# Optimization experiments

Hardware: AMD Instinct MI355X
Metric: run time of the kernel (lower is better)

## Reference

```python
import jax, jax.numpy as jnp
import numpy as np

H = 1024          # hidden_size
NH = 16           # num_heads = hidden_size // head_dim
DK = 64           # head_dim (key)
DV = 64           # head_v_dim
VDIM = 1024       # value_dim
DECAY_LR, GATE_LR, A_LR, V_LR = 64, 160, 64, 64
W_SCALE = -0.6065306597126334  # -exp(-0.5)
GN_EPS = 64 * 1e-5             # head_dim * norm_eps


def _lora(x, A, B, b, act):
    h = x @ A.T
    if act is not None:
        h = act(h)
    y = h @ B.T
    return y if b is None else y + b


def setup_inputs() -> dict:
    key = jax.random.key(0)
    ks = iter(jax.random.split(key, 40))
    def n(shape, s=0.02):
        return jax.random.normal(next(ks), shape, dtype=jnp.float32) * s
    inp = {
        'hidden_states': jax.random.normal(next(ks), (8, 2048, H), jnp.float32),
        'v_first': jax.random.normal(next(ks), (8, 2048, VDIM), jnp.float32),
        'x_r': n((1, 1, H), 0.5), 'x_w': n((1, 1, H), 0.5), 'x_k': n((1, 1, H), 0.5),
        'x_v': n((1, 1, H), 0.5), 'x_a': n((1, 1, H), 0.5), 'x_g': n((1, 1, H), 0.5),
        'k_k': 0.71 + n((H,), 0.05),
        'k_a': 1.02 + n((H,), 0.05),
        'r_k': -0.04 + n((NH, DK), 0.05),
        'W_r': n((H, H)), 'W_k': n((H, H)), 'W_v': n((VDIM, H)), 'W_o': n((H, VDIM)),
        'w_lora_A': n((DECAY_LR, H)), 'w_lora_B': n((H, DECAY_LR)), 'w_lora_b': n((H,), 0.5) - 4.0,
        'a_lora_A': n((A_LR, H)), 'a_lora_B': n((H, A_LR)), 'a_lora_b': n((H,), 0.1),
        'v_lora_A': n((V_LR, H)), 'v_lora_B': n((VDIM, V_LR)), 'v_lora_b': 0.73 + n((VDIM,), 0.1),
        'g_lora_A': n((GATE_LR, H)), 'g_lora_B': n((VDIM, GATE_LR)),
        'gn_w': jnp.ones((VDIM,), jnp.float32), 'gn_b': jnp.zeros((VDIM,), jnp.float32),
    }
    return inp


def reference(hidden_states, v_first, x_r, x_w, x_k, x_v, x_a, x_g, k_k, k_a, r_k,
              W_r, W_k, W_v, W_o, w_lora_A, w_lora_B, w_lora_b,
              a_lora_A, a_lora_B, a_lora_b, v_lora_A, v_lora_B, v_lora_b,
              g_lora_A, g_lora_B, gn_w, gn_b):
    x = hidden_states
    B_, T, _ = x.shape
    # token shift: delta[t] = x[t-1] - x[t], x[-1] = 0
    shifted = jnp.pad(x, ((0, 0), (1, 0), (0, 0)))[:, :T]
    delta = shifted - x
    xr = x + delta * x_r; xw = x + delta * x_w; xk = x + delta * x_k
    xv = x + delta * x_v; xa = x + delta * x_a; xg = x + delta * x_g

    r = xr @ W_r.T
    w = W_SCALE * jax.nn.sigmoid(_lora(xw, w_lora_A, w_lora_B, w_lora_b, jnp.tanh))  # log-decay in (-e^-0.5, 0)
    k = xk @ W_k.T
    v = xv @ W_v.T
    v = v + (v_first - v) * jax.nn.sigmoid(_lora(xv, v_lora_A, v_lora_B, v_lora_b, None))  # layer_idx != 0
    a = jax.nn.sigmoid(_lora(xa, a_lora_A, a_lora_B, a_lora_b, None))
    g = _lora(xg, g_lora_A, g_lora_B, None, jax.nn.sigmoid)

    kk = (k * k_k).reshape(B_, T, NH, DK)
    kk = kk / jnp.maximum(jnp.linalg.norm(kk, axis=-1, keepdims=True), 1e-12)  # l2 norm per head
    k = k * (1.0 + (a - 1.0) * k_a)

    rh = r.reshape(B_, T, NH, DK)
    wh = w.reshape(B_, T, NH, DK)
    kh = k.reshape(B_, T, NH, DK)
    vh = v.reshape(B_, T, NH, DV)
    ah = -kk                               # delta-rule 'a' (removal direction)
    bh = kk * a.reshape(B_, T, NH, DK)     # delta-rule 'b' (write direction)

    def step(S, inputs):
        # S: [B, H, DK, DV]; inputs each [B, H, D]
        r_t, w_t, k_t, v_t, a_t, b_t = inputs
        sa = jnp.einsum('bhk,bhkv->bhv', a_t, S)
        S = S * jnp.exp(w_t)[..., None] \
            + jnp.einsum('bhk,bhv->bhkv', b_t, sa) \
            + jnp.einsum('bhk,bhv->bhkv', k_t, v_t)
        o_t = jnp.einsum('bhk,bhkv->bhv', r_t, S)
        return S, o_t

    seq = tuple(jnp.moveaxis(t, 1, 0) for t in (rh, wh, kh, vh, ah, bh))  # [T,B,H,D]
    S0 = jnp.zeros((B_, NH, DK, DV), dtype=x.dtype)
    _, o = jax.lax.scan(step, S0, seq)
    o = jnp.moveaxis(o, 0, 1)  # [B, T, NH, DV]

    # GroupNorm with num_groups = num_heads over value_dim channels == per-head LayerNorm (no per-head affine)
    mu = o.mean(-1, keepdims=True)
    var = o.var(-1, keepdims=True)
    on = ((o - mu) / jnp.sqrt(var + GN_EPS)).reshape(B_, T, VDIM) * gn_w + gn_b

    bonus = ((rh * kh * r_k).sum(-1, keepdims=True) * vh).reshape(B_, T, VDIM)
    out = ((on + bonus) * g) @ W_o.T
    return out
```

## Files before the change

kernel.cpp:

```cpp
#include <hip/hip_runtime.h>
#include <hip/hip_bf16.h>


#define DEVI __device__ __forceinline__

constexpr int TSEQ = 2048;
constexpr int HID  = 1024;
constexpr int BTOT = 16384;
constexpr int CCH  = 32;
constexpr int NCH  = TSEQ / CCH;
constexpr float W_SCALE = -0.6065306597126334f;
constexpr float GN_EPS  = 6.4e-4f;

using s16x8  = __attribute__((ext_vector_type(8))) short;
using f32x4v = __attribute__((ext_vector_type(4))) float;

DEVI float4 ld4(const float* p) { return *reinterpret_cast<const float4*>(p); }
DEVI void   st4(float* p, float4 v) { *reinterpret_cast<float4*>(p) = v; }
DEVI float  sigf(float x) { return 1.0f / (1.0f + __expf(-x)); }
DEVI unsigned short bfr(float f) {
    unsigned int u = __float_as_uint(f);
    return (unsigned short)((u + 0x7fffu + ((u >> 16) & 1u)) >> 16);
}
DEVI float bff(unsigned short s) { return __uint_as_float(((unsigned int)s) << 16); }
DEVI unsigned int pk2(float lo, float hi) {
    return ((unsigned int)bfr(hi) << 16) | (unsigned int)bfr(lo);
}
DEVI f32x4v MF(s16x8 a, s16x8 b, f32x4v c) {
    return __builtin_amdgcn_mfma_f32_16x16x32_bf16(a, b, c, 0, 0, 0);
}
DEVI void gl16(const void* g, void* l) {
    __builtin_amdgcn_global_load_lds(
        (const __attribute__((address_space(1))) unsigned int*)g,
        (__attribute__((address_space(3))) unsigned int*)l, 16, 0, 0);
}
DEVI void gl4(const void* g, void* l) {
    __builtin_amdgcn_global_load_lds(
        (const __attribute__((address_space(1))) unsigned int*)g,
        (__attribute__((address_space(3))) unsigned int*)l, 4, 0, 0);
}

__global__ __launch_bounds__(256) void cast_kernel(
        const float* __restrict__ s, unsigned short* __restrict__ d, int n) {
    int i = (blockIdx.x * 256 + threadIdx.x) * 4;
    if (i >= n) return;
    float4 v = ld4(s + i);
    ushort4 o; o.x = bfr(v.x); o.y = bfr(v.y); o.z = bfr(v.z); o.w = bfr(v.w);
    *reinterpret_cast<ushort4*>(d + i) = o;
}

__global__ __launch_bounds__(256) void proj3_kernel(
        const float* __restrict__ x,
        const float* __restrict__ cr, const float* __restrict__ ck,
        const float* __restrict__ cv,
        const unsigned short* __restrict__ Wr, const unsigned short* __restrict__ Wk,
        const unsigned short* __restrict__ Wv,
        unsigned short* __restrict__ Ro, unsigned short* __restrict__ Ko,
        unsigned short* __restrict__ Vo) {
    __shared__ __align__(16) unsigned short As[3][64 * 32];
    __shared__ __align__(16) unsigned short Bs[3][128 * 32];
    const int tid = threadIdx.x;
    const int w = tid >> 6, l = tid & 63;
    const int bm = blockIdx.x * 64, bn = blockIdx.y * 128;
    const int wm = w >> 1, wn = w & 1;
    const int lr = l & 15, lq = l >> 4, lk = lq * 8;

    f32x4v acc[3][2][4];
#pragma unroll
    for (int p = 0; p < 3; p++)
#pragma unroll
        for (int i = 0; i < 2; i++)
#pragma unroll
            for (int j = 0; j < 4; j++)
#pragma unroll
                for (int q = 0; q < 4; q++) acc[p][i][j][q] = 0.f;

    const float* cvs[3] = {cr, ck, cv};
    const unsigned short* Ws[3] = {Wr, Wk, Wv};

    for (int k0 = 0; k0 < HID; k0 += 32) {
        {
            const int row = tid >> 2, kp = (tid & 3) * 8;
            const int gr = bm + row;
            const float* xp = x + (size_t)gr * HID + k0 + kp;
            float4 x0 = ld4(xp), x1 = ld4(xp + 4);
            float4 p0 = make_float4(0.f, 0.f, 0.f, 0.f), p1 = p0;
            if ((gr & (TSEQ - 1)) != 0) { p0 = ld4(xp - HID); p1 = ld4(xp - HID + 4); }
            float xb[8] = {x0.x, x0.y, x0.z, x0.w, x1.x, x1.y, x1.z, x1.w};
            float dx[8] = {p0.x - x0.x, p0.y - x0.y, p0.z - x0.z, p0.w - x0.w,
                           p1.x - x1.x, p1.y - x1.y, p1.z - x1.z, p1.w - x1.w};
#pragma unroll
            for (int p = 0; p < 3; p++) {
                float4 c0 = ld4(cvs[p] + k0 + kp), c1 = ld4(cvs[p] + k0 + kp + 4);
                float cc[8] = {c0.x, c0.y, c0.z, c0.w, c1.x, c1.y, c1.z, c1.w};
                uint4 u;
                u.x = pk2(fmaf(dx[0], cc[0], xb[0]), fmaf(dx[1], cc[1], xb[1]));
                u.y = pk2(fmaf(dx[2], cc[2], xb[2]), fmaf(dx[3], cc[3], xb[3]));
                u.z = pk2(fmaf(dx[4], cc[4], xb[4]), fmaf(dx[5], cc[5], xb[5]));
                u.w = pk2(fmaf(dx[6], cc[6], xb[6]), fmaf(dx[7], cc[7], xb[7]));
                *reinterpret_cast<uint4*>(&As[p][row * 32 + kp]) = u;
            }
        }
#pragma unroll
        for (int p = 0; p < 3; p++)
#pragma unroll
            for (int c = 0; c < 2; c++) {
                int idx = c * 256 + tid;
                int rw = idx >> 2, kp2 = (idx & 3) * 8;
                gl16(Ws[p] + (size_t)(bn + rw) * HID + k0 + kp2,
                     &Bs[p][c * 2048 + w * 512]);
            }
        __syncthreads();
#pragma unroll
        for (int p = 0; p < 3; p++) {
            s16x8 af[2], bf4[4];
#pragma unroll
            for (int i = 0; i < 2; i++)
                af[i] = *reinterpret_cast<const s16x8*>(
                    &As[p][(wm * 32 + i * 16 + lr) * 32 + lk]);
#pragma unroll
            for (int j = 0; j < 4; j++)
                bf4[j] = *reinterpret_cast<const s16x8*>(
                    &Bs[p][(wn * 64 + j * 16 + lr) * 32 + lk]);
#pragma unroll
            for (int i = 0; i < 2; i++)
#pragma unroll
                for (int j = 0; j < 4; j++)
                    acc[p][i][j] = MF(af[i], bf4[j], acc[p][i][j]);
        }
        __syncthreads();
    }

    unsigned short* dsts[3] = {Ro, Ko, Vo};
#pragma unroll
    for (int p = 0; p < 3; p++)
#pragma unroll
        for (int i = 0; i < 2; i++)
#pragma unroll
            for (int j = 0; j < 4; j++)
#pragma unroll
                for (int q = 0; q < 4; q++) {
                    const int grow = bm + wm * 32 + i * 16 + lq * 4 + q;
                    const int gcol = bn + wn * 64 + j * 16 + lr;
                    dsts[p][(size_t)grow * HID + gcol] = bfr(acc[p][i][j][q]);
                }
}

template<int BM, int BN, int MODE, bool MIXA, bool OUTBF>
__global__ __launch_bounds__(256) void mgemm(
        const void* __restrict__ Ap, const float* __restrict__ cvec,
        const unsigned short* __restrict__ Bw, void* Cout,
        int N, int K,
        const float* __restrict__ bias,
        const unsigned short* aux1, const float* __restrict__ aux2) {
    constexpr int BK = 32;
    constexpr int WM_ = (BN == 128) ? 2 : (BM == 128 ? 4 : 2);
    constexpr int WN_ = (BN == 128) ? 2 : (BM == 128 ? 1 : 2);
    constexpr int WTM = BM / WM_, WTN = BN / WN_;
    constexpr int MF_ = WTM / 16, NF = WTN / 16;
    constexpr int ACALLS = (BM * BK) / 2048;
    constexpr int BCALLS = (BN * BK) / 2048;
    __shared__ __align__(16) unsigned short As[BM * BK];
    __shared__ __align__(16) unsigned short Bs[BN * BK];
    const int tid = threadIdx.x;
    const int w = tid >> 6, l = tid & 63;
    const int bm = blockIdx.x * BM, bn = blockIdx.y * BN;
    const int wm = w / WN_, wn = w % WN_;
    const int lr = l & 15, lk = (l >> 4) * 8;

    f32x4v acc[MF_][NF];
#pragma unroll
    for (int i = 0; i < MF_; i++)
#pragma unroll
        for (int j = 0; j < NF; j++)
#pragma unroll
            for (int q = 0; q < 4; q++) acc[i][j][q] = 0.f;

    for (int k0 = 0; k0 < K; k0 += BK) {
        if (MIXA) {
            const float* Axf = (const float*)Ap;
#pragma unroll
            for (int c = 0; c < ACALLS; c++) {
                int idx = c * 256 + tid;
                int row = idx >> 2, kp = (idx & 3) * 8;
                int gr = bm + row;
                const float* xp = Axf + (size_t)gr * K + k0 + kp;
                float4 x0 = ld4(xp), x1 = ld4(xp + 4);
                float4 p0 = make_float4(0.f,0.f,0.f,0.f), p1 = p0;
                if ((gr & (TSEQ - 1)) != 0) { p0 = ld4(xp - HID); p1 = ld4(xp - HID + 4); }
                float4 c0 = ld4(cvec + k0 + kp), c1 = ld4(cvec + k0 + kp + 4);
                uint4 u;
                u.x = pk2(fmaf(p0.x - x0.x, c0.x, x0.x), fmaf(p0.y - x0.y, c0.y, x0.y));
                u.y = pk2(fmaf(p0.z - x0.z, c0.z, x0.z), fmaf(p0.w - x0.w, c0.w, x0.w));
                u.z = pk2(fmaf(p1.x - x1.x, c1.x, x1.x), fmaf(p1.y - x1.y, c1.y, x1.y));
                u.w = pk2(fmaf(p1.z - x1.z, c1.z, x1.z), fmaf(p1.w - x1.w, c1.w, x1.w));
                *reinterpret_cast<uint4*>(&As[idx * 8]) = u;
            }
        } else {
            const unsigned short* Ab = (const unsigned short*)Ap;
#pragma unroll
            for (int c = 0; c < ACALLS; c++) {
                int idx = c * 256 + tid;
                int row = idx >> 2, kp = (idx & 3) * 8;
                gl16(Ab + (size_t)(bm + row) * K + k0 + kp, &As[c * 2048 + w * 512]);
            }
        }
#pragma unroll
        for (int c = 0; c < BCALLS; c++) {
            int idx = c * 256 + tid;
            int row = idx >> 2, kp = (idx & 3) * 8;
            int gc = bn + row; if (gc > N - 1) gc = N - 1;
            gl16(Bw + (size_t)gc * K + k0 + kp, &Bs[c * 2048 + w * 512]);
        }
        __syncthreads();
        s16x8 afx[MF_], bfx[NF];
#pragma unroll
        for (int i = 0; i < MF_; i++)
            afx[i] = *reinterpret_cast<const s16x8*>(&As[(wm * WTM + i * 16 + lr) * BK + lk]);
#pragma unroll
        for (int j = 0; j < NF; j++)
            bfx[j] = *reinterpret_cast<const s16x8*>(&Bs[(wn * WTN + j * 16 + lr) * BK + lk]);
#pragma unroll
        for (int i = 0; i < MF_; i++)
#pragma unroll
            for (int j = 0; j < NF; j++)
                acc[i][j] = __builtin_amdgcn_mfma_f32_16x16x32_bf16(
                    afx[i], bfx[j], acc[i][j], 0, 0, 0);
        __syncthreads();
    }

#pragma unroll
    for (int i = 0; i < MF_; i++) {
        const int grow0 = bm + wm * WTM + i * 16 + (l >> 4) * 4;
#pragma unroll
        for (int j = 0; j < NF; j++) {
            const int gcol = bn + wn * WTN + j * 16 + lr;
            if (gcol >= N) continue;
            const float bsv = (MODE >= 3) ? bias[gcol] : 0.f;
#pragma unroll
            for (int q = 0; q < 4; q++) {
                const int grow = grow0 + q;
                float d = acc[i][j][q];
                if (MODE == 1) d = tanhf(d);
                else if (MODE == 2) d = sigf(d);
                else if (MODE == 3) d = __expf(W_SCALE * sigf(d + bsv));
                else if (MODE == 4) d = sigf(d + bsv);
                else if (MODE == 5) {
                    float v0 = bff(aux1[(size_t)grow * N + gcol]);
                    d = fmaf(aux2[(size_t)grow * N + gcol] - v0, sigf(d + bsv), v0);
                }
                else if (MODE == 6) d = W_SCALE * sigf(d + bsv);
                if (OUTBF) ((unsigned short*)Cout)[(size_t)grow * N + gcol] = bfr(d);
                else       ((float*)Cout)[(size_t)grow * N + gcol] = d;
            }
        }
    }
}

__global__ __launch_bounds__(64) void cprep_kernel(
        unsigned short* __restrict__ K16, unsigned short* __restrict__ A16,
        unsigned short* __restrict__ R16, unsigned short* __restrict__ KK16,
        const unsigned short* __restrict__ W16,
        const float* __restrict__ kkc, const float* __restrict__ kac,
        const float* __restrict__ rkw,
        float* __restrict__ SB, float* __restrict__ Ed,
        unsigned short* __restrict__ MvH, unsigned short* __restrict__ MvL) {
    __shared__ __align__(16) unsigned short sA[32][64], sB[32][64];
    __shared__ __align__(16) float Mab[32][36];
    const int bid = blockIdx.x;
    const int bh = bid >> 6, ch = bid & 63;
    const int bb = bh >> 4, hh = bh & 15;
    const int l = threadIdx.x;
    const int chn = hh * 64 + l;
    const float kkcv = kkc[chn], kacv = kac[chn], rkv = rkw[chn];
    size_t off = ((size_t)(bb * TSEQ) + ch * CCH) * HID + chn;
    float cw = 0.f, er = 1.f;
    for (int i = 0; i < CCH; i++, off += HID) {
        const float k = bff(K16[off]);
        const float a = bff(A16[off]);
        const float r = bff(R16[off]);
        const float wv = bff(W16[off]);
        const float kr = k * kkcv;
        float ss = kr * kr;
        ss += __shfl_xor(ss, 1);  ss += __shfl_xor(ss, 2);
        ss += __shfl_xor(ss, 4);  ss += __shfl_xor(ss, 8);
        ss += __shfl_xor(ss, 16); ss += __shfl_xor(ss, 32);
        const float inv = 1.0f / fmaxf(sqrtf(ss), 1e-12f);
        const float kk = kr * inv;
        const float b  = kk * a;
        const float kn = k * fmaf(a - 1.0f, kacv, 1.0f);
        float s3 = r * kn * rkv;
        s3 += __shfl_xor(s3, 1);  s3 += __shfl_xor(s3, 2);
        s3 += __shfl_xor(s3, 4);  s3 += __shfl_xor(s3, 8);
        s3 += __shfl_xor(s3, 16); s3 += __shfl_xor(s3, 32);
        if (l == 0) SB[(size_t)bh * TSEQ + ch * CCH + i] = s3;
        const float cwp = cw; cw += wv;
        const float ea = __expf(cwp), ei = __expf(-cw);
        er = __expf(cw);
        const unsigned short At = bfr(-kk * ea);
        const unsigned short Bt = bfr(b * ei);
        KK16[off] = At;
        A16[off]  = Bt;
        K16[off]  = bfr(kn * ei);
        R16[off]  = bfr(r * er);
        sA[i][l] = At; sB[i][l] = Bt;
    }
    Ed[((size_t)bh * NCH + ch) * 64 + l] = er;
    __syncthreads();
    const int lr = l & 15, lq = l >> 4;
    f32x4v z4; z4[0] = z4[1] = z4[2] = z4[3] = 0.f;
#pragma unroll
    for (int mi = 0; mi < 2; mi++)
#pragma unroll
        for (int ni = 0; ni < 2; ni++) {
            s16x8 a0 = *reinterpret_cast<const s16x8*>(&sA[mi * 16 + lr][lq * 8]);
            s16x8 a1 = *reinterpret_cast<const s16x8*>(&sA[mi * 16 + lr][32 + lq * 8]);
            s16x8 b0 = *reinterpret_cast<const s16x8*>(&sB[ni * 16 + lr][lq * 8]);
            s16x8 b1 = *reinterpret_cast<const s16x8*>(&sB[ni * 16 + lr][32 + lq * 8]);
            f32x4v m = MF(a1, b1, MF(a0, b0, z4));
#pragma unroll
            for (int q = 0; q < 4; q++) {
                int r = mi * 16 + lq * 4 + q, cc2 = ni * 16 + lr;
                Mab[r][cc2] = (cc2 < r) ? m[q] : 0.f;
            }
        }
    __syncthreads();
    const int j = l & 31;
    float m[32];
#pragma unroll
    for (int i = 0; i < 32; i++) m[i] = (i == j) ? 1.f : 0.f;
#pragma unroll
    for (int i = 1; i < 32; i++) {
        float p0 = 0.f, p1 = 0.f, p2 = 0.f, p3 = 0.f;
#pragma unroll
        for (int k4_ = 0; k4_ < 32; k4_ += 4) {
            if (k4_ >= i) break;
            float4 L4 = *reinterpret_cast<const float4*>(&Mab[i][k4_]);
            p0 = fmaf(L4.x, m[k4_ + 0], p0);
            if (k4_ + 1 < i) p1 = fmaf(L4.y, m[k4_ + 1], p1);
            if (k4_ + 2 < i) p2 = fmaf(L4.z, m[k4_ + 2], p2);
            if (k4_ + 3 < i) p3 = fmaf(L4.w, m[k4_ + 3], p3);
        }
        m[i] += (p0 + p1) + (p2 + p3);
    }
    if (l < 32) {
        unsigned short* dH = MvH + (size_t)(bh * NCH + ch) * 1024;
        unsigned short* dL = MvL + (size_t)(bh * NCH + ch) * 1024;
#pragma unroll
        for (int i = 0; i < 32; i++) {
            unsigned short h = bfr(m[i]);
            dH[i * 32 + j] = h;
            dL[i * 32 + j] = bfr(m[i] - bff(h));
        }
    }
}

__global__ __launch_bounds__(256) void recchunk_kernel(
        const unsigned short* __restrict__ AtG, const unsigned short* __restrict__ BtG,
        const unsigned short* __restrict__ KtG, const unsigned short* __restrict__ RtG,
        const unsigned short* __restrict__ V16, const float* __restrict__ Ed,
        const unsigned short* __restrict__ MvH, const unsigned short* __restrict__ MvL,
        float* __restrict__ Ob) {
    __shared__ __align__(16) unsigned short stT[2][4][CCH][64];
    __shared__ __align__(16) unsigned short stMh[2][32][32], stMl[2][32][32];
    __shared__ __align__(16) unsigned short stV[2][CCH][16];
    __shared__ __align__(16) float stEd[2][64];
    __shared__ __align__(16) unsigned short Shi[16][74], Slo[16][74];
    __shared__ __align__(16) unsigned short BtT[64][42], KtT[64][42];
    __shared__ __align__(16) unsigned short VT[16][42];
    __shared__ __align__(16) unsigned short MakH[32][42], MakL[32][42];
    __shared__ __align__(16) unsigned short MrkH[32][42], MrkL[32][42];
    __shared__ __align__(16) unsigned short MrbH[32][42], MrbL[32][42];
    __shared__ __align__(16) unsigned short rhTH[16][42], rhTL[16][42];

    const int bid = blockIdx.x;
    const int vq = bid >> 7, bh = bid & 127;
    const int tid = threadIdx.x;
    const int w = tid >> 6, l = tid & 63;
    const int lr = l & 15, lq = l >> 4;
    const int bb = bh >> 4, hh = bh & 15;
    const size_t rowoff = ((size_t)bb * TSEQ) * HID + hh * 64;
    const int mi = w >> 1, ni = w & 1;

    const int r8 = l >> 3, ck = l & 7;
    const int swz8 = (ck ^ r8) * 8;

    auto STAGE = [&](int buf, int cn) {
        if (cn >= NCH) return;
        const size_t cb = rowoff + (size_t)(cn * CCH) * HID;
        const unsigned short* srcs[4] = {AtG, BtG, KtG, RtG};
        const unsigned short* T = srcs[w];
#pragma unroll
        for (int c = 0; c < 4; c++)
            gl16(T + cb + (size_t)(c * 8 + r8) * HID + swz8, &stT[buf][w][c * 8][0]);
        if (w == 0) {
            gl16(V16 + cb + (size_t)(l >> 1) * HID + vq * 16 + (l & 1) * 8,
                 &stV[buf][0][0]);
            gl4(Ed + ((size_t)bh * NCH + cn) * 64 + l, &stEd[buf][0]);
        } else if (w == 1) {
#pragma unroll
            for (int c = 0; c < 2; c++)
                gl16(MvH + (size_t)(bh * NCH + cn) * 1024 + c * 512 + l * 8,
                     (char*)&stMh[buf][0][0] + c * 1024);
        } else if (w == 2) {
#pragma unroll
            for (int c = 0; c < 2; c++)
                gl16(MvL + (size_t)(bh * NCH + cn) * 1024 + c * 512 + l * 8,
                     (char*)&stMl[buf][0][0] + c * 1024);
        }
    };

    for (int idx = tid; idx < 16 * 74; idx += 256) {
        ((unsigned short*)Shi)[idx] = 0;
        ((unsigned short*)Slo)[idx] = 0;
    }
    STAGE(0, 0);
    asm volatile("s_waitcnt vmcnt(0)" ::: "memory");
    __syncthreads();

    auto fragT = [&](int bf, int tn, int rbase, int kb) -> s16x8 {
        int row = rbase + lr;
        int chv = ((kb >> 3) + lq) ^ (row & 7);
        return *reinterpret_cast<const s16x8*>(
            (const char*)&stT[bf][tn][0][0] + row * 128 + chv * 16);
    };
    auto fragS = [&](const unsigned short (*Sx)[74], int kb) -> s16x8 {
        return *reinterpret_cast<const s16x8*>(&Sx[lr][kb + lq * 8]);
    };
    auto frag42 = [&](const unsigned short (*T)[42], int rbase) -> s16x8 {
        return *reinterpret_cast<const s16x8*>(&T[rbase + lr][lq * 8]);
    };

    f32x4v Sacc;
#pragma unroll
    for (int q = 0; q < 4; q++) Sacc[q] = 0.f;
    f32x4v z4; z4[0] = z4[1] = z4[2] = z4[3] = 0.f;

    int buf = 0;
    for (int c = 0; c < NCH; c++) {
        STAGE(buf ^ 1, c + 1);
        {
            const int tt = tid & 31, g8 = tid >> 5;
            const int ch = g8 ^ (tt & 7);
            uint4 bu = *reinterpret_cast<const uint4*>(&stT[buf][1][tt][ch * 8]);
            uint4 ku = *reinterpret_cast<const uint4*>(&stT[buf][2][tt][ch * 8]);
            unsigned int bw[4] = {bu.x, bu.y, bu.z, bu.w};
            unsigned int kw[4] = {ku.x, ku.y, ku.z, ku.w};
#pragma unroll
            for (int e = 0; e < 4; e++) {
                BtT[g8 * 8 + 2 * e][tt]     = (unsigned short)(bw[e] & 0xffffu);
                BtT[g8 * 8 + 2 * e + 1][tt] = (unsigned short)(bw[e] >> 16);
                KtT[g8 * 8 + 2 * e][tt]     = (unsigned short)(kw[e] & 0xffffu);
                KtT[g8 * 8 + 2 * e + 1][tt] = (unsigned short)(kw[e] >> 16);
            }
            if (g8 < 4) {
                ushort4 vu = *reinterpret_cast<const ushort4*>(&stV[buf][tt][g8 * 4]);
                VT[g8 * 4 + 0][tt] = vu.x; VT[g8 * 4 + 1][tt] = vu.y;
                VT[g8 * 4 + 2][tt] = vu.z; VT[g8 * 4 + 3][tt] = vu.w;
            }
        }
        s16x8 atm0 = fragT(buf, 0, mi * 16, 0), atm1 = fragT(buf, 0, mi * 16, 32);
        s16x8 rt0  = fragT(buf, 3, mi * 16, 0), rt1  = fragT(buf, 3, mi * 16, 32);
        s16x8 bt0  = fragT(buf, 1, ni * 16, 0), bt1  = fragT(buf, 1, ni * 16, 32);
        s16x8 kt0  = fragT(buf, 2, ni * 16, 0), kt1  = fragT(buf, 2, ni * 16, 32);
        f32x4v mak = MF(atm1, kt1, MF(atm0, kt0, z4));
        f32x4v mrk = MF(rt1, kt1, MF(rt0, kt0, z4));
        f32x4v mrb = MF(rt1, bt1, MF(rt0, bt0, z4));
        f32x4v oac = z4, rhT = z4;
        {
            s16x8 sh0 = fragS(Shi, 0), sh1 = fragS(Shi, 32);
            s16x8 sl0 = fragS(Slo, 0), sl1 = fragS(Slo, 32);
            if (ni == 0) {
                oac = MF(rt1, sl1, MF(rt0, sl0, MF(rt1, sh1, MF(rt0, sh0, z4))));
            } else {
                rhT = MF(sl1, atm1, MF(sl0, atm0, MF(sh1, atm1, MF(sh0, atm0, z4))));
            }
        }
#pragma unroll
        for (int q = 0; q < 4; q++) {
            const int r = mi * 16 + lq * 4 + q, cc = ni * 16 + lr;
            float vv = (cc < r) ? mak[q] : 0.f;
            unsigned short h = bfr(vv);
            MakH[r][cc] = h; MakL[r][cc] = bfr(vv - bff(h));
            vv = (cc <= r) ? mrk[q] : 0.f; h = bfr(vv);
            MrkH[r][cc] = h; MrkL[r][cc] = bfr(vv - bff(h));
            vv = (cc <= r) ? mrb[q] : 0.f; h = bfr(vv);
            MrbH[r][cc] = h; MrbL[r][cc] = bfr(vv - bff(h));
        }
        __syncthreads();
        {
            s16x8 vt0 = frag42(VT, 0);
            if (ni == 0) {
                oac = MF(frag42(MrkL, mi * 16), vt0,
                         MF(frag42(MrkH, mi * 16), vt0, oac));
            } else {
                rhT = MF(vt0, frag42(MakL, mi * 16),
                         MF(vt0, frag42(MakH, mi * 16), rhT));
#pragma unroll
                for (int q = 0; q < 4; q++) {
                    const int r = lq * 4 + q, cc = mi * 16 + lr;
                    unsigned short h = bfr(rhT[q]);
                    rhTH[r][cc] = h; rhTL[r][cc] = bfr(rhT[q] - bff(h));
                }
            }
        }
        __syncthreads();
        if (ni == 1) {
            s16x8 rh0 = frag42(rhTH, 0), rl0 = frag42(rhTL, 0);
            s16x8 mvh = *reinterpret_cast<const s16x8*>(&stMh[buf][mi * 16 + lr][lq * 8]);
            s16x8 mvl = *reinterpret_cast<const s16x8*>(&stMl[buf][mi * 16 + lr][lq * 8]);
            f32x4v sat = MF(rl0, mvh, MF(rh0, mvl, MF(rh0, mvh, z4)));
#pragma unroll
            for (int q = 0; q < 4; q++) {
                const int r = lq * 4 + q, cc = mi * 16 + lr;
                unsigned short h = bfr(sat[q]);
                MakH[r][cc] = h;
                MakL[r][cc] = bfr(sat[q] - bff(h));
            }
        }
        __syncthreads();
        {
            s16x8 sath = frag42(MakH, 0), satl = frag42(MakL, 0);
            if (ni == 0) {
                s16x8 rbh = frag42(MrbH, mi * 16), rbl = frag42(MrbL, mi * 16);
                oac = MF(rbl, sath, MF(rbh, satl, MF(rbh, sath, oac)));
#pragma unroll
                for (int q = 0; q < 4; q++) {
                    const int t = c * CCH + mi * 16 + lq * 4 + q;
                    Ob[rowoff + (size_t)t * HID + vq * 16 + lr] = oac[q];
                }
            }
            s16x8 btf = frag42(BtT, w * 16);
            s16x8 ktf = frag42(KtT, w * 16);
            s16x8 vta = frag42(VT, 0);
            const float ed = stEd[buf][w * 16 + lr];
            Sacc = MF(sath, btf, Sacc);
            Sacc = MF(satl, btf, Sacc);
            Sacc = MF(vta, ktf, Sacc);
#pragma unroll
            for (int q = 0; q < 4; q++) {
                Sacc[q] *= ed;
                unsigned short h = bfr(Sacc[q]);
                Shi[lq * 4 + q][w * 16 + lr] = h;
                Slo[lq * 4 + q][w * 16 + lr] = bfr(Sacc[q] - bff(h));
            }
        }
        asm volatile("s_waitcnt vmcnt(0)" ::: "memory");
        __syncthreads();
        buf ^= 1;
    }
}

__global__ __launch_bounds__(256) void post_kernel(
        const float* __restrict__ Ob, const unsigned short* __restrict__ V16,
        const float* __restrict__ G, const float* __restrict__ SB,
        const float* __restrict__ gnw, const float* __restrict__ gnb,
        unsigned short* __restrict__ Y16) {
    const int row = blockIdx.x;
    const int tid = threadIdx.x;
    const int c   = tid * 4;
    const size_t off = (size_t)row * HID + c;
    float4 o4 = ld4(Ob + off), g4 = ld4(G + off);
    ushort4 vu = *reinterpret_cast<const ushort4*>(V16 + off);
    float v[4]  = {bff(vu.x), bff(vu.y), bff(vu.z), bff(vu.w)};
    const int hh = tid >> 4;
    const int bb = row >> 11, t = row & (TSEQ - 1);
    const float s3 = SB[((size_t)(bb * 16 + hh)) * TSEQ + t];

    float s1 = o4.x + o4.y + o4.z + o4.w;
    float s2 = o4.x*o4.x + o4.y*o4.y + o4.z*o4.z + o4.w*o4.w;
#pragma unroll
    for (int m = 1; m < 16; m <<= 1) {
        s1 += __shfl_xor(s1, m); s2 += __shfl_xor(s2, m);
    }
    const float mu  = s1 * (1.0f / 64.0f);
    const float var = s2 * (1.0f / 64.0f) - mu * mu;
    const float inv = rsqrtf(var + GN_EPS);
    float4 gw = ld4(gnw + c), gb = ld4(gnb + c);
    ushort4 y;
    y.x = bfr((fmaf((o4.x - mu) * inv, gw.x, gb.x) + s3 * v[0]) * g4.x);
    y.y = bfr((fmaf((o4.y - mu) * inv, gw.y, gb.y) + s3 * v[1]) * g4.y);
    y.z = bfr((fmaf((o4.z - mu) * inv, gw.z, gb.z) + s3 * v[2]) * g4.z);
    y.w = bfr((fmaf((o4.w - mu) * inv, gw.w, gb.w) + s3 * v[3]) * g4.w);
    *reinterpret_cast<ushort4*>(Y16 + off) = y;
}

extern "C" void kernel_launch(void* const* d_in, const int* in_sizes, int n_in,
                              void* d_out, int out_size, void* d_ws, size_t ws_size,
                              hipStream_t stream) {
    const float* x   = (const float*)d_in[0];
    const float* vf  = (const float*)d_in[1];
    const float* x_r = (const float*)d_in[2];
    const float* x_w = (const float*)d_in[3];
    const float* x_k = (const float*)d_in[4];
    const float* x_v = (const float*)d_in[5];
    const float* x_a = (const float*)d_in[6];
    const float* x_g = (const float*)d_in[7];
    const float* k_k = (const float*)d_in[8];
    const float* k_a = (const float*)d_in[9];
    const float* r_k = (const float*)d_in[10];
    const float* W_r = (const float*)d_in[11];
    const float* W_k = (const float*)d_in[12];
    const float* W_v = (const float*)d_in[13];
    const float* W_o = (const float*)d_in[14];
    const float* wA  = (const float*)d_in[15];
    const float* wB  = (const float*)d_in[16];
    const float* wb  = (const float*)d_in[17];
    const float* aA  = (const float*)d_in[18];
    const float* aB  = (const float*)d_in[19];
    const float* ab  = (const float*)d_in[20];
    const float* vA  = (const float*)d_in[21];
    const float* vB  = (const float*)d_in[22];
    const float* vb  = (const float*)d_in[23];
    const float* gA  = (const float*)d_in[24];
    const float* gB  = (const float*)d_in[25];
    const float* gnw = (const float*)d_in[26];
    const float* gnb = (const float*)d_in[27];
    float* out = (float*)d_out;

    float* ws = (float*)d_ws;
    const size_t SZ = (size_t)BTOT * HID;
    const size_t HH = (size_t)HID * HID;
    float*          REG  = ws;
    unsigned short* P    = (unsigned short*)(ws + SZ);
    unsigned short* R16  = P;
    unsigned short* K16  = P + 1 * SZ;
    unsigned short* V16  = P + 2 * SZ;
    unsigned short* A16  = P + 3 * SZ;
    unsigned short* KK16 = P + 4 * SZ;
    unsigned short* H1   = P + 5 * SZ;
    unsigned short* WR   = H1 + (size_t)BTOT * 160;
    unsigned short* Wr16 = WR;
    unsigned short* Wk16 = WR + 1 * HH;
    unsigned short* Wv16 = WR + 2 * HH;
    unsigned short* Wo16 = WR + 3 * HH;
    unsigned short* wA16 = WR + 4 * HH;
    unsigned short* wB16 = wA16 + 65536;
    unsigned short* aA16 = wB16 + 65536;
    unsigned short* aB16 = aA16 + 65536;
    unsigned short* vA16 = aB16 + 65536;
    unsigned short* vB16 = vA16 + 65536;
    unsigned short* gA16 = vB16 + 65536;
    unsigned short* gB16 = gA16 + 163840;
    float*          SB   = (float*)(gB16 + 163840);
    float*          Ed   = SB + (size_t)128 * TSEQ;
    unsigned short* W16   = (unsigned short*)REG;
    unsigned short* MinvH = (unsigned short*)(REG + 8 * 1024 * 1024);
    unsigned short* MinvL = MinvH + (size_t)128 * NCH * 1024;
    unsigned short* Y16  = R16;
    float*          G    = REG;

    const dim3 blk(256);
    const dim3 gBig(128, 8);
    const dim3 gP3(BTOT / 64, 8);
    const dim3 gL64(256, 1);
    const dim3 gL160(256, 3);
    const float* np = nullptr;
    const unsigned short* nu = nullptr;

    auto CAST = [&](const float* s, unsigned short* d, int n) {
        cast_kernel<<<dim3((n / 4 + 255) / 256), blk, 0, stream>>>(s, d, n);
    };
    CAST(W_r, Wr16, (int)HH); CAST(W_k, Wk16, (int)HH);
    CAST(W_v, Wv16, (int)HH); CAST(W_o, Wo16, (int)HH);
    CAST(wA, wA16, 65536); CAST(wB, wB16, 65536);
    CAST(aA, aA16, 65536); CAST(aB, aB16, 65536);
    CAST(vA, vA16, 65536); CAST(vB, vB16, 65536);
    CAST(gA, gA16, 163840); CAST(gB, gB16, 163840);

    proj3_kernel<<<gP3, blk, 0, stream>>>(
        x, x_r, x_k, x_v, Wr16, Wk16, Wv16, R16, K16, V16);
    mgemm<64,64,0,true,true><<<gL64, blk, 0, stream>>>(
        x, x_v, vA16, H1, 64, HID, np, nu, np);
    mgemm<128,128,5,false,true><<<gBig, blk, 0, stream>>>(
        H1, np, vB16, V16, HID, 64, vb, V16, vf);
    mgemm<64,64,1,true,true><<<gL64, blk, 0, stream>>>(
        x, x_w, wA16, H1, 64, HID, np, nu, np);
    mgemm<128,128,6,false,true><<<gBig, blk, 0, stream>>>(
        H1, np, wB16, W16, HID, 64, wb, nu, np);
    mgemm<64,64,0,true,true><<<gL64, blk, 0, stream>>>(
        x, x_a, aA16, H1, 64, HID, np, nu, np);
    mgemm<128,128,4,false,true><<<gBig, blk, 0, stream>>>(
        H1, np, aB16, A16, HID, 64, ab, nu, np);
    cprep_kernel<<<dim3(128 * NCH), dim3(64), 0, stream>>>(
        K16, A16, R16, KK16, W16, k_k, k_a, r_k, SB, Ed, MinvH, MinvL);
    recchunk_kernel<<<dim3(512), blk, 0, stream>>>(
        KK16, A16, K16, R16, V16, Ed, MinvH, MinvL, out);
    mgemm<64,64,2,true,true><<<gL160, blk, 0, stream>>>(
        x, x_g, gA16, H1, 160, HID, np, nu, np);
    mgemm<128,128,0,false,false><<<gBig, blk, 0, stream>>>(
        H1, np, gB16, G, HID, 160, np, nu, np);
    post_kernel<<<dim3(BTOT), blk, 0, stream>>>(
        out, V16, G, SB, gnw, gnb, Y16);
    mgemm<128,128,0,false,false><<<gBig, blk, 0, stream>>>(
        Y16, np, Wo16, out, HID, HID, np, nu, np);
    (void)in_sizes; (void)n_in; (void)out_size; (void)ws_size;
}
```

Baseline: 1.140 ms.

## Fuse four LoRA down-projections into one kernel and store gate as bf16

A new lora4 kernel computes the token-shift mixes for the v, w, a and g branches from a single read of x. It multiplies them against one concatenated 352-row bf16 LoRA-A weight, applies the per-branch activations (tanh, sigmoid), and writes one packed H1 buffer. The up-projection GEMMs then read their slice of H1 through a new lda stride. This replaces four separate MIXA GEMM launches that each reloaded x and its shifted row. The gate output G is now stored as bf16 instead of fp32, halving its write and read traffic in post_kernel at the cost of some precision on the gate.

```diff
diff --git a/kernel.cpp b/kernel.cpp
--- a/kernel.cpp
+++ b/kernel.cpp
@@ -9,6 +9,7 @@
 constexpr int BTOT = 16384;
 constexpr int CCH  = 32;
 constexpr int NCH  = TSEQ / CCH;
+constexpr int L4N  = 352;
 constexpr float W_SCALE = -0.6065306597126334f;
 constexpr float GN_EPS  = 6.4e-4f;
 
@@ -146,16 +147,92 @@
                 }
 }
 
-template<int BM, int BN, int MODE, bool MIXA, bool OUTBF>
+__global__ __launch_bounds__(256) void lora4_kernel(
+        const float* __restrict__ x,
+        const float* __restrict__ cv_, const float* __restrict__ cw_,
+        const float* __restrict__ ca_, const float* __restrict__ cg_,
+        const unsigned short* __restrict__ LW, unsigned short* __restrict__ H1) {
+    __shared__ __align__(16) unsigned short As[4][64 * 32];
+    __shared__ __align__(16) unsigned short Bs[L4N * 32];
+    const int tid = threadIdx.x;
+    const int w = tid >> 6, l = tid & 63;
+    const int lr = l & 15, lq = l >> 4, lk = lq * 8;
+    const int bm = blockIdx.x * 64;
+    const float* cvs[4] = {cv_, cw_, ca_, cg_};
+
+    f32x4v acc[22];
+#pragma unroll
+    for (int j = 0; j < 22; j++)
+#pragma unroll
+        for (int q = 0; q < 4; q++) acc[j][q] = 0.f;
+
+    for (int k0 = 0; k0 < HID; k0 += 32) {
+        {
+            const int row = tid >> 2, kp = (tid & 3) * 8;
+            const int gr = bm + row;
+            const float* xp = x + (size_t)gr * HID + k0 + kp;
+            float4 x0 = ld4(xp), x1 = ld4(xp + 4);
+            float4 p0 = make_float4(0.f, 0.f, 0.f, 0.f), p1 = p0;
+            if ((gr & (TSEQ - 1)) != 0) { p0 = ld4(xp - HID); p1 = ld4(xp - HID + 4); }
+            float xb[8] = {x0.x, x0.y, x0.z, x0.w, x1.x, x1.y, x1.z, x1.w};
+            float dx[8] = {p0.x - x0.x, p0.y - x0.y, p0.z - x0.z, p0.w - x0.w,
+                           p1.x - x1.x, p1.y - x1.y, p1.z - x1.z, p1.w - x1.w};
+#pragma unroll
+            for (int p = 0; p < 4; p++) {
+                float4 c0 = ld4(cvs[p] + k0 + kp), c1 = ld4(cvs[p] + k0 + kp + 4);
+                float cc[8] = {c0.x, c0.y, c0.z, c0.w, c1.x, c1.y, c1.z, c1.w};
+                uint4 u;
+                u.x = pk2(fmaf(dx[0], cc[0], xb[0]), fmaf(dx[1], cc[1], xb[1]));
+                u.y = pk2(fmaf(dx[2], cc[2], xb[2]), fmaf(dx[3], cc[3], xb[3]));
+                u.z = pk2(fmaf(dx[4], cc[4], xb[4]), fmaf(dx[5], cc[5], xb[5]));
+                u.w = pk2(fmaf(dx[6], cc[6], xb[6]), fmaf(dx[7], cc[7], xb[7]));
+                *reinterpret_cast<uint4*>(&As[p][row * 32 + kp]) = u;
+            }
+        }
+#pragma unroll
+        for (int c = 0; c < 6; c++) {
+            int idx = c * 256 + tid;
+            if (idx < L4N * 4) {
+                gl16(LW + (size_t)(idx >> 2) * HID + (idx & 3) * 8 + k0,
+                     (char*)&Bs[0] + (c * 256 + w * 64) * 16);
+            }
+        }
+        __syncthreads();
+        s16x8 af[4];
+#pragma unroll
+        for (int p = 0; p < 4; p++)
+            af[p] = *reinterpret_cast<const s16x8*>(&As[p][(w * 16 + lr) * 32 + lk]);
+#pragma unroll
+        for (int j = 0; j < 22; j++) {
+            const int grp = (j < 4) ? 0 : (j < 8) ? 1 : (j < 12) ? 2 : 3;
+            s16x8 bf = *reinterpret_cast<const s16x8*>(&Bs[(j * 16 + lr) * 32 + lk]);
+            acc[j] = MF(af[grp], bf, acc[j]);
+        }
+        __syncthreads();
+    }
+
+#pragma unroll
+    for (int j = 0; j < 22; j++)
+#pragma unroll
+        for (int q = 0; q < 4; q++) {
+            const int grow = bm + w * 16 + lq * 4 + q;
+            const int gcol = j * 16 + lr;
+            float d = acc[j][q];
+            if (j >= 4 && j < 8) d = tanhf(d);
+            else if (j >= 12) d = sigf(d);
+            H1[(size_t)grow * L4N + gcol] = bfr(d);
+        }
+}
+
+template<int BM, int BN, int MODE, bool OUTBF>
 __global__ __launch_bounds__(256) void mgemm(
-        const void* __restrict__ Ap, const float* __restrict__ cvec,
-        const unsigned short* __restrict__ Bw, void* Cout,
-        int N, int K,
+        const unsigned short* __restrict__ Ab, const unsigned short* __restrict__ Bw,
+        void* Cout, int N, int K, int lda,
         const float* __restrict__ bias,
         const unsigned short* aux1, const float* __restrict__ aux2) {
     constexpr int BK = 32;
-    constexpr int WM_ = (BN == 128) ? 2 : (BM == 128 ? 4 : 2);
-    constexpr int WN_ = (BN == 128) ? 2 : (BM == 128 ? 1 : 2);
+    constexpr int WM_ = (BN == 128) ? 2 : 4;
+    constexpr int WN_ = (BN == 128) ? 2 : 1;
     constexpr int WTM = BM / WM_, WTN = BN / WN_;
     constexpr int MF_ = WTM / 16, NF = WTN / 16;
     constexpr int ACALLS = (BM * BK) / 2048;
@@ -177,33 +254,11 @@
             for (int q = 0; q < 4; q++) acc[i][j][q] = 0.f;
 
     for (int k0 = 0; k0 < K; k0 += BK) {
-        if (MIXA) {
-            const float* Axf = (const float*)Ap;
-#pragma unroll
-            for (int c = 0; c < ACALLS; c++) {
-                int idx = c * 256 + tid;
-                int row = idx >> 2, kp = (idx & 3) * 8;
-                int gr = bm + row;
-                const float* xp = Axf + (size_t)gr * K + k0 + kp;
-                float4 x0 = ld4(xp), x1 = ld4(xp + 4);
-                float4 p0 = make_float4(0.f,0.f,0.f,0.f), p1 = p0;
-                if ((gr & (TSEQ - 1)) != 0) { p0 = ld4(xp - HID); p1 = ld4(xp - HID + 4); }
-                float4 c0 = ld4(cvec + k0 + kp), c1 = ld4(cvec + k0 + kp + 4);
-                uint4 u;
-                u.x = pk2(fmaf(p0.x - x0.x, c0.x, x0.x), fmaf(p0.y - x0.y, c0.y, x0.y));
-                u.y = pk2(fmaf(p0.z - x0.z, c0.z, x0.z), fmaf(p0.w - x0.w, c0.w, x0.w));
-                u.z = pk2(fmaf(p1.x - x1.x, c1.x, x1.x), fmaf(p1.y - x1.y, c1.y, x1.y));
-                u.w = pk2(fmaf(p1.z - x1.z, c1.z, x1.z), fmaf(p1.w - x1.w, c1.w, x1.w));
-                *reinterpret_cast<uint4*>(&As[idx * 8]) = u;
-            }
-        } else {
-            const unsigned short* Ab = (const unsigned short*)Ap;
-#pragma unroll
-            for (int c = 0; c < ACALLS; c++) {
-                int idx = c * 256 + tid;
-                int row = idx >> 2, kp = (idx & 3) * 8;
-                gl16(Ab + (size_t)(bm + row) * K + k0 + kp, &As[c * 2048 + w * 512]);
-            }
+#pragma unroll
+        for (int c = 0; c < ACALLS; c++) {
+            int idx = c * 256 + tid;
+            int row = idx >> 2, kp = (idx & 3) * 8;
+            gl16(Ab + (size_t)(bm + row) * lda + k0 + kp, &As[c * 2048 + w * 512]);
         }
 #pragma unroll
         for (int c = 0; c < BCALLS; c++) {
@@ -236,15 +291,12 @@
         for (int j = 0; j < NF; j++) {
             const int gcol = bn + wn * WTN + j * 16 + lr;
             if (gcol >= N) continue;
-            const float bsv = (MODE >= 3) ? bias[gcol] : 0.f;
+            const float bsv = (MODE >= 4) ? bias[gcol] : 0.f;
 #pragma unroll
             for (int q = 0; q < 4; q++) {
                 const int grow = grow0 + q;
                 float d = acc[i][j][q];
-                if (MODE == 1) d = tanhf(d);
-                else if (MODE == 2) d = sigf(d);
-                else if (MODE == 3) d = __expf(W_SCALE * sigf(d + bsv));
-                else if (MODE == 4) d = sigf(d + bsv);
+                if (MODE == 4) d = sigf(d + bsv);
                 else if (MODE == 5) {
                     float v0 = bff(aux1[(size_t)grow * N + gcol]);
                     d = fmaf(aux2[(size_t)grow * N + gcol] - v0, sigf(d + bsv), v0);
@@ -553,16 +605,18 @@
 
 __global__ __launch_bounds__(256) void post_kernel(
         const float* __restrict__ Ob, const unsigned short* __restrict__ V16,
-        const float* __restrict__ G, const float* __restrict__ SB,
+        const unsigned short* __restrict__ G16, const float* __restrict__ SB,
         const float* __restrict__ gnw, const float* __restrict__ gnb,
         unsigned short* __restrict__ Y16) {
     const int row = blockIdx.x;
     const int tid = threadIdx.x;
     const int c   = tid * 4;
     const size_t off = (size_t)row * HID + c;
-    float4 o4 = ld4(Ob + off), g4 = ld4(G + off);
+    float4 o4 = ld4(Ob + off);
     ushort4 vu = *reinterpret_cast<const ushort4*>(V16 + off);
-    float v[4]  = {bff(vu.x), bff(vu.y), bff(vu.z), bff(vu.w)};
+    ushort4 gu = *reinterpret_cast<const ushort4*>(G16 + off);
+    float v[4] = {bff(vu.x), bff(vu.y), bff(vu.z), bff(vu.w)};
+    float g[4] = {bff(gu.x), bff(gu.y), bff(gu.z), bff(gu.w)};
     const int hh = tid >> 4;
     const int bb = row >> 11, t = row & (TSEQ - 1);
     const float s3 = SB[((size_t)(bb * 16 + hh)) * TSEQ + t];
@@ -578,10 +632,10 @@
     const float inv = rsqrtf(var + GN_EPS);
     float4 gw = ld4(gnw + c), gb = ld4(gnb + c);
     ushort4 y;
-    y.x = bfr((fmaf((o4.x - mu) * inv, gw.x, gb.x) + s3 * v[0]) * g4.x);
-    y.y = bfr((fmaf((o4.y - mu) * inv, gw.y, gb.y) + s3 * v[1]) * g4.y);
-    y.z = bfr((fmaf((o4.z - mu) * inv, gw.z, gb.z) + s3 * v[2]) * g4.z);
-    y.w = bfr((fmaf((o4.w - mu) * inv, gw.w, gb.w) + s3 * v[3]) * g4.w);
+    y.x = bfr((fmaf((o4.x - mu) * inv, gw.x, gb.x) + s3 * v[0]) * g[0]);
+    y.y = bfr((fmaf((o4.y - mu) * inv, gw.y, gb.y) + s3 * v[1]) * g[1]);
+    y.z = bfr((fmaf((o4.z - mu) * inv, gw.z, gb.z) + s3 * v[2]) * g[2]);
+    y.w = bfr((fmaf((o4.w - mu) * inv, gw.w, gb.w) + s3 * v[3]) * g[3]);
     *reinterpret_cast<ushort4*>(Y16 + off) = y;
 }
 
@@ -629,70 +683,61 @@
     unsigned short* A16  = P + 3 * SZ;
     unsigned short* KK16 = P + 4 * SZ;
     unsigned short* H1   = P + 5 * SZ;
-    unsigned short* WR   = H1 + (size_t)BTOT * 160;
+    unsigned short* WR   = H1 + (size_t)BTOT * L4N;
     unsigned short* Wr16 = WR;
     unsigned short* Wk16 = WR + 1 * HH;
     unsigned short* Wv16 = WR + 2 * HH;
     unsigned short* Wo16 = WR + 3 * HH;
-    unsigned short* wA16 = WR + 4 * HH;
-    unsigned short* wB16 = wA16 + 65536;
-    unsigned short* aA16 = wB16 + 65536;
-    unsigned short* aB16 = aA16 + 65536;
-    unsigned short* vA16 = aB16 + 65536;
-    unsigned short* vB16 = vA16 + 65536;
-    unsigned short* gA16 = vB16 + 65536;
-    unsigned short* gB16 = gA16 + 163840;
+    unsigned short* LW   = WR + 4 * HH;
+    unsigned short* vB16 = LW + (size_t)L4N * HID;
+    unsigned short* wB16 = vB16 + 65536;
+    unsigned short* aB16 = wB16 + 65536;
+    unsigned short* gB16 = aB16 + 65536;
     float*          SB   = (float*)(gB16 + 163840);
     float*          Ed   = SB + (size_t)128 * TSEQ;
     unsigned short* W16   = (unsigned short*)REG;
     unsigned short* MinvH = (unsigned short*)(REG + 8 * 1024 * 1024);
     unsigned short* MinvL = MinvH + (size_t)128 * NCH * 1024;
     unsigned short* Y16  = R16;
-    float*          G    = REG;
+    unsigned short* G16  = (unsigned short*)REG;
 
     const dim3 blk(256);
     const dim3 gBig(128, 8);
     const dim3 gP3(BTOT / 64, 8);
-    const dim3 gL64(256, 1);
-    const dim3 gL160(256, 3);
+    const unsigned short* nu = nullptr;
     const float* np = nullptr;
-    const unsigned short* nu = nullptr;
 
     auto CAST = [&](const float* s, unsigned short* d, int n) {
         cast_kernel<<<dim3((n / 4 + 255) / 256), blk, 0, stream>>>(s, d, n);
     };
     CAST(W_r, Wr16, (int)HH); CAST(W_k, Wk16, (int)HH);
     CAST(W_v, Wv16, (int)HH); CAST(W_o, Wo16, (int)HH);
-    CAST(wA, wA16, 65536); CAST(wB, wB16, 65536);
-    CAST(aA, aA16, 65536); CAST(aB, aB16, 65536);
-    CAST(vA, vA16, 65536); CAST(vB, vB16, 65536);
-    CAST(gA, gA16, 163840); CAST(gB, gB16, 163840);
+    CAST(vA, LW + 0 * 65536, 65536);
+    CAST(wA, LW + 1 * 65536, 65536);
+    CAST(aA, LW + 2 * 65536, 65536);
+    CAST(gA, LW + 3 * 65536, 163840);
+    CAST(vB, vB16, 65536); CAST(wB, wB16, 65536);
+    CAST(aB, aB16, 65536); CAST(gB, gB16, 163840);
 
     proj3_kernel<<<gP3, blk, 0, stream>>>(
         x, x_r, x_k, x_v, Wr16, Wk16, Wv16, R16, K16, V16);
-    mgemm<64,64,0,true,true><<<gL64, blk, 0, stream>>>(
-        x, x_v, vA16, H1, 64, HID, np, nu, np);
-    mgemm<128,128,5,false,true><<<gBig, blk, 0, stream>>>(
-        H1, np, vB16, V16, HID, 64, vb, V16, vf);
-    mgemm<64,64,1,true,true><<<gL64, blk, 0, stream>>>(
-        x, x_w, wA16, H1, 64, HID, np, nu, np);
-    mgemm<128,128,6,false,true><<<gBig, blk, 0, stream>>>(
-        H1, np, wB16, W16, HID, 64, wb, nu, np);
-    mgemm<64,64,0,true,true><<<gL64, blk, 0, stream>>>(
-        x, x_a, aA16, H1, 64, HID, np, nu, np);
-    mgemm<128,128,4,false,true><<<gBig, blk, 0, stream>>>(
-        H1, np, aB16, A16, HID, 64, ab, nu, np);
+    lora4_kernel<<<dim3(BTOT / 64), blk, 0, stream>>>(
+        x, x_v, x_w, x_a, x_g, LW, H1);
+    mgemm<128,128,5,true><<<gBig, blk, 0, stream>>>(
+        H1 + 0, vB16, V16, HID, 64, L4N, vb, V16, vf);
+    mgemm<128,128,6,true><<<gBig, blk, 0, stream>>>(
+        H1 + 64, wB16, W16, HID, 64, L4N, wb, nu, np);
+    mgemm<128,128,4,true><<<gBig, blk, 0, stream>>>(
+        H1 + 128, aB16, A16, HID, 64, L4N, ab, nu, np);
     cprep_kernel<<<dim3(128 * NCH), dim3(64), 0, stream>>>(
         K16, A16, R16, KK16, W16, k_k, k_a, r_k, SB, Ed, MinvH, MinvL);
     recchunk_kernel<<<dim3(512), blk, 0, stream>>>(
         KK16, A16, K16, R16, V16, Ed, MinvH, MinvL, out);
-    mgemm<64,64,2,true,true><<<gL160, blk, 0, stream>>>(
-        x, x_g, gA16, H1, 160, HID, np, nu, np);
-    mgemm<128,128,0,false,false><<<gBig, blk, 0, stream>>>(
-        H1, np, gB16, G, HID, 160, np, nu, np);
+    mgemm<128,128,0,true><<<gBig, blk, 0, stream>>>(
+        H1 + 192, gB16, G16, HID, 160, L4N, np, nu, np);
     post_kernel<<<dim3(BTOT), blk, 0, stream>>>(
-        out, V16, G, SB, gnw, gnb, Y16);
-    mgemm<128,128,0,false,false><<<gBig, blk, 0, stream>>>(
-        Y16, np, Wo16, out, HID, HID, np, nu, np);
+        out, V16, G16, SB, gnw, gnb, Y16);
+    mgemm<128,128,0,false><<<gBig, blk, 0, stream>>>(
+        Y16, Wo16, out, HID, HID, HID, np, nu, np);
     (void)in_sizes; (void)n_in; (void)out_size; (void)ws_size;
 }
```

Result: faster. 1.051 ms (-7.8%).
